# Optimization experiments

Hardware: AMD Instinct MI355X
Metric: run time of the kernel (lower is better)

Reference implementation:

```python
import jax, jax.numpy as jnp
import numpy as np

B_, S_, D_ = 2, 1024, 1024
EXPAND = 2
D_INNER = EXPAND * D_            # 2048
HEADDIM = 64
NHEADS = D_INNER // HEADDIM      # 32
D_STATE = 64
NGROUPS = 1
D_CONV = 4
CONV_DIM = D_INNER + 2 * NGROUPS * D_STATE      # 2176
D_IN_PROJ = 2 * D_INNER + 2 * NGROUPS * D_STATE + NHEADS  # 4256
H_MLP = 8 * D_                   # GatedMLP fc_1 out (scale * d_model)


def setup_inputs() -> dict:
    key = jax.random.key(0)
    ks = jax.random.split(key, 12)
    n = lambda k, shp, s=0.02: jax.random.normal(k, shp, dtype=jnp.float32) * s
    return {
        "x": jax.random.normal(ks[0], (B_, S_, D_), dtype=jnp.float32),
        "in_proj_w": n(ks[1], (D_IN_PROJ, D_)),
        "conv_w": n(ks[2], (CONV_DIM, D_CONV), 0.2),
        "conv_b": jnp.zeros((CONV_DIM,), jnp.float32),
        "dt_bias": jax.random.normal(ks[3], (NHEADS,), dtype=jnp.float32) * 0.5 - 2.0,
        "A_log": jnp.log(1.0 + 15.0 * jax.random.uniform(ks[4], (NHEADS,), dtype=jnp.float32)),
        "D": jax.random.normal(ks[5], (NHEADS,), dtype=jnp.float32) * 0.1 + 1.0,
        "ssm_norm_w": jnp.ones((D_INNER,), jnp.float32),
        "out_proj_w": n(ks[6], (D_, D_INNER)),
        "rms_w": jnp.ones((D_,), jnp.float32),
        "fc1_w": n(ks[7], (H_MLP, D_)),
        "fc2_w": n(ks[8], (D_, H_MLP // 2)),
    }


def _rms(x, w, eps=1e-5):
    return x * jax.lax.rsqrt(jnp.mean(x * x, axis=-1, keepdims=True) + eps) * w


def _mamba(x, in_proj_w, conv_w, conv_b, dt_bias, A_log, D, ssm_norm_w, out_proj_w):
    b, s, _ = x.shape
    zxbcdt = x @ in_proj_w.T                         # [b,s,D_IN_PROJ]
    z = zxbcdt[..., :D_INNER]
    xBC = zxbcdt[..., D_INNER:D_INNER + CONV_DIM]
    dt_raw = zxbcdt[..., -NHEADS:]
    # causal depthwise conv1d + SiLU
    xc = jnp.pad(jnp.transpose(xBC, (0, 2, 1)), ((0, 0), (0, 0), (D_CONV - 1, 0)))
    xc = jax.lax.conv_general_dilated(xc, conv_w[:, None, :], (1,), 'VALID',
                                      feature_group_count=CONV_DIM,
                                      dimension_numbers=('NCH', 'OIH', 'NCH'))
    xBC = jax.nn.silu(jnp.transpose(xc, (0, 2, 1)) + conv_b)
    xs = xBC[..., :D_INNER].reshape(b, s, NHEADS, HEADDIM)
    Bm = xBC[..., D_INNER:D_INNER + D_STATE]         # [b,s,n] (ngroups=1)
    Cm = xBC[..., D_INNER + D_STATE:]
    dt = jax.nn.softplus(dt_raw + dt_bias)           # [b,s,h]
    dA = jnp.exp(dt * (-jnp.exp(A_log)))             # [b,s,h]
    dtx = dt[..., None] * xs                          # [b,s,h,p]

    def step(h, inp):
        dA_t, dtx_t, B_t, C_t = inp
        h = h * dA_t[:, :, None, None] + jnp.einsum('bhp,bn->bhpn', dtx_t, B_t)
        y = jnp.einsum('bhpn,bn->bhp', h, C_t)
        return h, y

    h0 = jnp.zeros((b, NHEADS, HEADDIM, D_STATE), x.dtype)
    _, y = jax.lax.scan(step, h0, (jnp.transpose(dA, (1, 0, 2)),
                                   jnp.transpose(dtx, (1, 0, 2, 3)),
                                   jnp.transpose(Bm, (1, 0, 2)),
                                   jnp.transpose(Cm, (1, 0, 2))))
    y = jnp.transpose(y, (1, 0, 2, 3)) + D[None, None, :, None] * xs
    y = y.reshape(b, s, D_INNER) * jax.nn.silu(z)    # gated
    y = _rms(y, ssm_norm_w)
    return y @ out_proj_w.T


def reference(x, in_proj_w, conv_w, conv_b, dt_bias, A_log, D, ssm_norm_w,
              out_proj_w, rms_w, fc1_w, fc2_w):
    # x = x + mamba(x)
    x = x + _mamba(x, in_proj_w, conv_w, conv_b, dt_bias, A_log, D, ssm_norm_w, out_proj_w)
    # x = x + GatedMLP(RMSNorm(x))
    xn = _rms(x, rms_w)
    h1 = xn @ fc1_w.T
    a, g = jnp.split(h1, 2, axis=-1)
    m = (a * jax.nn.silu(g)) @ fc2_w.T
    return x + m
```

## Files before the change

### kernel.cpp

```cpp
#include <hip/hip_runtime.h>
#include <math.h>

typedef unsigned short u16;
typedef __attribute__((ext_vector_type(8))) __bf16 bf16x8;
typedef __attribute__((ext_vector_type(4))) float f32x4;
typedef __attribute__((ext_vector_type(4))) u16 u16x4;
typedef __attribute__((ext_vector_type(8))) u16 u16x8;
typedef __attribute__((ext_vector_type(4))) float float4v;

constexpr int kS = 1024;
constexpr int kD = 1024;
constexpr int kDinner = 2048;
constexpr int kHeads = 32;
constexpr int kConvDim = 2176;
constexpr int kDproj = 4256;
constexpr int kDprojPad = 4352;
constexpr int kRows = 2048;
constexpr int kHmlp = 8192;
constexpr int kHhalf = 4096;
constexpr int kL = 64;
constexpr int kNC = 16;

__device__ __forceinline__ float bf2f(u16 u) {
    return __builtin_bit_cast(float, (unsigned int)u << 16);
}
__device__ __forceinline__ u16 f2bf(float f) {
    unsigned int u = __builtin_bit_cast(unsigned int, f);
    u += 0x7fffu + ((u >> 16) & 1u);
    return (u16)(u >> 16);
}
__device__ __forceinline__ float silu_(float x) { return x / (1.f + __expf(-x)); }

__device__ __forceinline__ void gld16(const u16* g, u16* l) {
    __builtin_amdgcn_global_load_lds(
        (const __attribute__((address_space(1))) void*)g,
        (__attribute__((address_space(3))) void*)l, 16, 0, 0);
}

constexpr int kB1 = kRows * kD / 4;
constexpr int kB2 = kB1 + kDprojPad * kD / 4;
constexpr int kB3 = kB2 + kD * kDinner / 4;
constexpr int kB4 = kB3 + kHmlp * kD / 4;
constexpr int kB5 = kB4 + kD * kHhalf / 4;
__global__ __launch_bounds__(256)
void cast_all_kernel(const float* __restrict__ x, const float* __restrict__ w1,
                     const float* __restrict__ w2, const float* __restrict__ w3,
                     const float* __restrict__ w4, u16* __restrict__ xbf,
                     u16* __restrict__ w1bf, u16* __restrict__ w2bf,
                     u16* __restrict__ w3bf, u16* __restrict__ w4bf) {
    int i = blockIdx.x * 256 + threadIdx.x;
    const float* src;
    u16* dst;
    int j;
    if (i < kB1) {
        j = i; src = x; dst = xbf;
    } else if (i < kB2) {
        j = i - kB1;
        int e = j * 4, row = e >> 10, col = e & 1023;
        u16x4 o = {0, 0, 0, 0};
        if (row < kDproj) {
            float4v v = *(const float4v*)(w1 + (size_t)row * kD + col);
            o.x = f2bf(v.x); o.y = f2bf(v.y); o.z = f2bf(v.z); o.w = f2bf(v.w);
        }
        ((u16x4*)w1bf)[j] = o;
        return;
    } else if (i < kB3) {
        j = i - kB2; src = w2; dst = w2bf;
    } else if (i < kB4) {
        j = i - kB3;
        int e = j * 4, row = e >> 10, col4 = (e & 1023) >> 2;
        int p = (row < kHhalf) ? row : row - kHhalf;
        int permrow = (p >> 4) * 32 + (p & 15) + ((row < kHhalf) ? 0 : 16);
        float4v v = ((const float4v*)w3)[j];
        u16x4 o;
        o.x = f2bf(v.x); o.y = f2bf(v.y); o.z = f2bf(v.z); o.w = f2bf(v.w);
        ((u16x4*)w3bf)[permrow * 256 + col4] = o;
        return;
    } else {
        j = i - kB4; src = w4; dst = w4bf;
    }
    float4v v = ((const float4v*)src)[j];
    u16x4 o;
    o.x = f2bf(v.x); o.y = f2bf(v.y); o.z = f2bf(v.z); o.w = f2bf(v.w);
    ((u16x4*)dst)[j] = o;
}

template <bool OUT_BF16, bool GATED = false>
__global__ __launch_bounds__(256)
void gemm_bt(const u16* __restrict__ A, const u16* __restrict__ W,
             void* __restrict__ Cout, const float* __restrict__ resid,
             int M, int N, int K) {
    __shared__ u16 As[2][128 * 32];
    __shared__ u16 Bs[2][128 * 32];
    const int tid = threadIdx.x;
    const int lane = tid & 63;
    const int w = __builtin_amdgcn_readfirstlane(tid >> 6);
    const int wm = w >> 1, wn = w & 1;
    const int bm = blockIdx.y * 128;
    const int bn = blockIdx.x * 128;
    const int z = blockIdx.z;
    const int Kchunk = K / gridDim.z;
    const int k0 = z * Kchunk;

    f32x4 acc[4][4];
#pragma unroll
    for (int i = 0; i < 4; i++)
#pragma unroll
        for (int j = 0; j < 4; j++) acc[i][j] = {0.f, 0.f, 0.f, 0.f};

    const int srow = lane >> 2;
    const int scol = (lane & 3) * 8;
    const u16* gA = A + (size_t)(bm + w * 32 + srow) * K + k0 + scol;
    const u16* gB = W + (size_t)(bn + w * 32 + srow) * K + k0 + scol;
    const size_t rstep = (size_t)16 * K;

    const int sbase0 = (w * 32) * 32;
    const int sbase1 = (w * 32 + 16) * 32;
    const int fra = (lane & 15) * 32 + (lane >> 4) * 8;

    gld16(gA, &As[0][sbase0]);
    gld16(gA + rstep, &As[0][sbase1]);
    gld16(gB, &Bs[0][sbase0]);
    gld16(gB + rstep, &Bs[0][sbase1]);

    const int nk = Kchunk >> 5;
    for (int i = 0; i < nk; i++) {
        const int cur = i & 1, nxt = cur ^ 1;
        __syncthreads();
        if (i + 1 < nk) {
            int kt2 = (i + 1) * 32;
            gld16(gA + kt2, &As[nxt][sbase0]);
            gld16(gA + kt2 + rstep, &As[nxt][sbase1]);
            gld16(gB + kt2, &Bs[nxt][sbase0]);
            gld16(gB + kt2 + rstep, &Bs[nxt][sbase1]);
        }
        bf16x8 av[4], bv[4];
#pragma unroll
        for (int mi = 0; mi < 4; mi++)
            av[mi] = *(const bf16x8*)&As[cur][(wm * 64 + mi * 16) * 32 + fra];
#pragma unroll
        for (int ni = 0; ni < 4; ni++)
            bv[ni] = *(const bf16x8*)&Bs[cur][(wn * 64 + ni * 16) * 32 + fra];
#pragma unroll
        for (int mi = 0; mi < 4; mi++)
#pragma unroll
            for (int ni = 0; ni < 4; ni++)
                acc[mi][ni] = __builtin_amdgcn_mfma_f32_16x16x32_bf16(av[mi], bv[ni], acc[mi][ni], 0, 0, 0);
    }

    const int rb = bm + wm * 64 + ((lane >> 4) << 2);
    const int cb = bn + wn * 64 + (lane & 15);
    if (GATED) {
        u16* Cb = (u16*)Cout;
        const int NG = N >> 1;
        const int gc0 = ((bn + wn * 64) >> 1) + (lane & 15);
#pragma unroll
        for (int mi = 0; mi < 4; mi++) {
#pragma unroll
            for (int p = 0; p < 2; p++) {
#pragma unroll
                for (int r = 0; r < 4; r++) {
                    float a = acc[mi][2 * p][r];
                    float g = acc[mi][2 * p + 1][r];
                    Cb[(size_t)(rb + mi * 16 + r) * NG + gc0 + p * 16] =
                        f2bf(a * silu_(g));
                }
            }
        }
        return;
    }
    float* Cf = (float*)Cout + (size_t)z * M * N;
    u16* Cb = (u16*)Cout;
#pragma unroll
    for (int mi = 0; mi < 4; mi++) {
#pragma unroll
        for (int ni = 0; ni < 4; ni++) {
#pragma unroll
            for (int r = 0; r < 4; r++) {
                size_t offo = (size_t)(rb + mi * 16 + r) * N + (cb + ni * 16);
                float v = acc[mi][ni][r];
                if (resid) v += resid[offo];
                if (OUT_BF16) Cb[offo] = f2bf(v);
                else Cf[offo] = v;
            }
        }
    }
}

#define VMCNT6 asm volatile("s_waitcnt vmcnt(6)" ::: "memory")
#define VMCNT0 asm volatile("s_waitcnt vmcnt(0)" ::: "memory")

__global__ __launch_bounds__(512, 2)
void gemm256_gated(const u16* __restrict__ A, const u16* __restrict__ W,
                   u16* __restrict__ Cout, int M, int N, int K) {
    __shared__ u16 lds[2][2][2][2][4096];
    const int tid = threadIdx.x;
    const int lane = tid & 63;
    const int w = __builtin_amdgcn_readfirstlane(tid >> 6);
    const int wm = w >> 2;
    const int wn = w & 3;
    const int wnh = wn >> 1, wnl = wn & 1;

    const int lin = blockIdx.x;
    const int xcd = lin & 7, j = lin >> 3;
    const int bm = (((xcd >> 2) << 2) + (j & 3)) << 8;
    const int bn = (((xcd & 3) << 3) + (j >> 2)) << 8;

    const int rst = tid >> 2, sst = tid & 3;
    const int vst = (((rst >> 1) & 1) << 1) | ((rst >> 2) & 1);
    const u16* gA0 = A + (size_t)(bm + rst) * K + ((sst ^ vst) << 3);
    const u16* gB0 = W + (size_t)(bn + rst) * K + ((sst ^ vst) << 3);
    const size_t hstep = (size_t)128 * K;
    const int wq512 = w * 512;

    const int r0a = lane & 15, slot = lane >> 4;
    const int v2a = (((r0a >> 1) & 1) << 1) | ((r0a >> 2) & 1);
    const int fro = r0a * 32 + ((slot ^ v2a) << 3);

    f32x4 acc[8][4];
#pragma unroll
    for (int i = 0; i < 8; i++)
#pragma unroll
        for (int j_ = 0; j_ < 4; j_++) acc[i][j_] = {0.f, 0.f, 0.f, 0.f};
    bf16x8 bv[4];
    const int nt = K >> 6;

#define STAGE(d, mat, kh, kt)                                               \
    { const u16* g_ = ((mat) ? gB0 : gA0) + (size_t)(kt) * 64 + (kh) * 32;  \
      gld16(g_, &lds[d][mat][0][kh][wq512]);                                \
      gld16(g_ + hstep, &lds[d][mat][1][kh][wq512]); }

#define LDA_FRAG(dst, d, kh, mfb)                                           \
    _Pragma("unroll") for (int i_ = 0; i_ < 4; i_++)                        \
        dst[i_] = *(const bf16x8*)&lds[d][0][wm][kh][((mfb) + i_) * 512 + fro];

#define LDB_FRAG(d, kh)                                                     \
    _Pragma("unroll") for (int i_ = 0; i_ < 4; i_++)                        \
        bv[i_] = *(const bf16x8*)&lds[d][1][wnh][kh][wnl * 2048 + i_ * 512 + fro];

#define PHASE_TAIL(g4, ...)                                                 \
    __builtin_amdgcn_s_barrier();                                           \
    asm volatile("s_waitcnt lgkmcnt(0)" ::: "memory");                      \
    __builtin_amdgcn_s_setprio(1);                                          \
    _Pragma("unroll") for (int i_ = 0; i_ < 4; i_++)                        \
        _Pragma("unroll") for (int n_ = 0; n_ < 4; n_++)                    \
            acc[(g4) * 4 + i_][n_] = __builtin_amdgcn_mfma_f32_16x16x32_bf16( \
                av[i_], bv[n_], acc[(g4) * 4 + i_][n_], 0, 0, 0);           \
    __builtin_amdgcn_s_setprio(0);                                          \
    __VA_ARGS__;                                                            \
    __builtin_amdgcn_s_barrier();

#define TILE(T, D)                                                          \
    {                                             \
      { bf16x8 av[4]; LDB_FRAG(D, 0); LDA_FRAG(av, D, 0, 0);                \
        if ((T) + 1 < nt) STAGE(D ^ 1, 0, 1, (T) + 1);                      \
        PHASE_TAIL(0, ((void)0)) }                                          \
                                                  \
      { bf16x8 av[4]; LDA_FRAG(av, D, 0, 4);                                \
        if ((T) + 2 < nt) STAGE(D, 1, 0, (T) + 2);                          \
        PHASE_TAIL(1, ((void)0)) }                                          \
                                                  \
      { bf16x8 av[4]; LDB_FRAG(D, 1); LDA_FRAG(av, D, 1, 0);                \
        if ((T) + 2 < nt) STAGE(D, 0, 0, (T) + 2);                          \
        PHASE_TAIL(0, ((void)0)) }                                          \
                \
      { bf16x8 av[4]; LDA_FRAG(av, D, 1, 4);                                \
        if ((T) + 2 < nt) STAGE(D, 1, 1, (T) + 2);                          \
        PHASE_TAIL(1, if ((T) + 2 < nt) { VMCNT6; }                         \
                      else if ((T) + 1 < nt) { VMCNT0; }) }                 \
    }

    STAGE(0, 1, 0, 0);
    STAGE(0, 0, 0, 0);
    STAGE(0, 1, 1, 0);
    STAGE(0, 0, 1, 0);
    STAGE(1, 1, 0, 1);
    STAGE(1, 0, 0, 1);
    STAGE(1, 1, 1, 1);
    VMCNT6;
    __builtin_amdgcn_s_barrier();

    for (int tt = 0; tt < nt; tt += 2) {
        TILE(tt, 0)
        TILE(tt + 1, 1)
    }

#undef TILE
#undef PHASE_TAIL
#undef LDB_FRAG
#undef LDA_FRAG
#undef STAGE

    __syncthreads();
    u16* cst = (u16*)&lds[0][0][0][0][0];
    constexpr int LDE = 136;
#pragma unroll
    for (int mf = 0; mf < 8; mf++) {
#pragma unroll
        for (int p = 0; p < 2; p++) {
#pragma unroll
            for (int r = 0; r < 4; r++) {
                float a = acc[mf][2 * p][r];
                float g = acc[mf][2 * p + 1][r];
                cst[(wm * 128 + mf * 16 + slot * 4 + r) * LDE +
                    wn * 32 + p * 16 + r0a] = f2bf(a * silu_(g));
            }
        }
    }
    __syncthreads();
    const int NG = N >> 1;
#pragma unroll
    for (int k = 0; k < 8; k++) {
        int ch = k * 512 + tid;
        int row = ch >> 4, c8 = (ch & 15) * 8;
        *(u16x8*)(Cout + (size_t)(bm + row) * NG + (bn >> 1) + c8) =
            *(const u16x8*)&cst[row * LDE + c8];
    }
}

__global__ __launch_bounds__(256)
void splitk_reduce_kernel(const float* __restrict__ Cp, const float* __restrict__ resid,
                          float* __restrict__ out, int mn4) {
    int i = blockIdx.x * 256 + threadIdx.x;
    if (i >= mn4) return;
    constexpr size_t MN = (size_t)kRows * kD;
    float4v s0 = ((const float4v*)Cp)[i];
    float4v s1 = ((const float4v*)(Cp + MN))[i];
    float4v s2 = ((const float4v*)(Cp + 2 * MN))[i];
    float4v s3 = ((const float4v*)(Cp + 3 * MN))[i];
    float4v r = ((const float4v*)resid)[i];
    float4v o;
    o.x = s0.x + s1.x + s2.x + s3.x + r.x;
    o.y = s0.y + s1.y + s2.y + s3.y + r.y;
    o.z = s0.z + s1.z + s2.z + s3.z + r.z;
    o.w = s0.w + s1.w + s2.w + s3.w + r.w;
    ((float4v*)out)[i] = o;
}

__global__ __launch_bounds__(256)
void reduce_rms_kernel(const float* __restrict__ Cp, const float* __restrict__ resid,
                       float* __restrict__ x2, const float* __restrict__ rmsw,
                       u16* __restrict__ xnbf) {
    const int row = blockIdx.x;
    const int tid = threadIdx.x;
    constexpr size_t MN = (size_t)kRows * kD;
    size_t i = (size_t)row * (kD / 4) + tid;
    float4v s0 = ((const float4v*)Cp)[i];
    float4v s1 = ((const float4v*)(Cp + MN))[i];
    float4v s2 = ((const float4v*)(Cp + 2 * MN))[i];
    float4v s3 = ((const float4v*)(Cp + 3 * MN))[i];
    float4v r = ((const float4v*)resid)[i];
    float4v v;
    v.x = s0.x + s1.x + s2.x + s3.x + r.x;
    v.y = s0.y + s1.y + s2.y + s3.y + r.y;
    v.z = s0.z + s1.z + s2.z + s3.z + r.z;
    v.w = s0.w + s1.w + s2.w + s3.w + r.w;
    ((float4v*)x2)[i] = v;
    float ss = v.x * v.x + v.y * v.y + v.z * v.z + v.w * v.w;
#pragma unroll
    for (int off = 32; off > 0; off >>= 1) ss += __shfl_down(ss, off);
    __shared__ float red[4];
    int wv = tid >> 6, lane = tid & 63;
    if (lane == 0) red[wv] = ss;
    __syncthreads();
    ss = red[0] + red[1] + red[2] + red[3];
    float rstd = rsqrtf(ss * (1.f / kD) + 1e-5f);
    float4v wv4 = ((const float4v*)rmsw)[tid];
    u16x4 o;
    o.x = f2bf(v.x * rstd * wv4.x);
    o.y = f2bf(v.y * rstd * wv4.y);
    o.z = f2bf(v.z * rstd * wv4.z);
    o.w = f2bf(v.w * rstd * wv4.w);
    ((u16x4*)xnbf)[i] = o;
}

__global__ __launch_bounds__(256)
void convdt_kernel(const u16* __restrict__ zxbf, const float* __restrict__ convw,
                   const float* __restrict__ convb, u16* __restrict__ xsbf,
                   float* __restrict__ BCf, const float* __restrict__ dt_bias,
                   float* __restrict__ dtf) {
    int c = blockIdx.x * 256 + threadIdx.x;
    int row = blockIdx.y;
    if (c >= kConvDim + kHeads) return;
    if (c < kConvDim) {
        int s = row & (kS - 1);
        float acc = convb[c];
#pragma unroll
        for (int j = 0; j < 4; j++) {
            int sj = s - 3 + j;
            if (sj >= 0)
                acc += bf2f(zxbf[(size_t)(row - 3 + j) * kDprojPad + kDinner + c]) * convw[c * 4 + j];
        }
        float v = silu_(acc);
        if (c < kDinner) xsbf[(size_t)row * kDinner + c] = f2bf(v);
        else BCf[(size_t)row * 128 + (c - kDinner)] = v;
    } else {
        int h = c - kConvDim;
        float raw = bf2f(zxbf[(size_t)row * kDprojPad + (kDinner + kConvDim) + h]) + dt_bias[h];
        float dt = (raw > 20.f) ? raw : log1pf(__expf(raw));
        dtf[(size_t)row * kHeads + h] = dt;
    }
}

__global__ __launch_bounds__(256)
void scan_chunk_kernel(const u16* __restrict__ xsbf, const float* __restrict__ BCf,
                       const float* __restrict__ dtf, const float* __restrict__ A_log,
                       const float* __restrict__ Dv, u16* __restrict__ ysbf,
                       float* __restrict__ Pf, float* __restrict__ Scf) {
    constexpr int LDT = 72;
    __shared__ __align__(16) char smem[65280];
    u16* Chi  = (u16*)(smem);
    u16* Clo  = (u16*)(smem + 9216);
    u16* Bhi  = (u16*)(smem + 18432);
    u16* Blo  = (u16*)(smem + 27648);
    u16* BThi = (u16*)(smem + 36864);
    u16* BTlo = (u16*)(smem + 46080);
    u16* xT   = (u16*)(smem + 55296);
    float* laS  = (float*)(smem + 64512);
    float* dtS  = (float*)(smem + 64768);
    float* wscS = (float*)(smem + 65024);
    u16* Mhi  = Clo;
    u16* Mlo  = Bhi;
    u16* ybuf = Chi;

    const int c = blockIdx.x, h = blockIdx.y, b = blockIdx.z;
    const int tid = threadIdx.x;
    const int lane = tid & 63;
    const int w = __builtin_amdgcn_readfirstlane(tid >> 6);
    const int row0 = b * kS + c * kL;
    const int frow = lane & 15;
    const int fk = (lane >> 4) * 8;
    const int q4 = (lane >> 4) * 4;
    const int w16 = w * 16;

#pragma unroll
    for (int k = 0; k < 8; k++) {
        int e4 = k * 256 + tid;
        int t = e4 >> 5, col = (e4 & 31) * 4;
        float4v v = *(const float4v*)(BCf + (size_t)(row0 + t) * 128 + col);
        u16x4 hi, lo;
        hi.x = f2bf(v.x); lo.x = f2bf(v.x - bf2f(hi.x));
        hi.y = f2bf(v.y); lo.y = f2bf(v.y - bf2f(hi.y));
        hi.z = f2bf(v.z); lo.z = f2bf(v.z - bf2f(hi.z));
        hi.w = f2bf(v.w); lo.w = f2bf(v.w - bf2f(hi.w));
        int cc = col & 63;
        u16* dh = (col < 64) ? Bhi : Chi;
        u16* dl = (col < 64) ? Blo : Clo;
        *(u16x4*)&dh[t * LDT + cc] = hi;
        *(u16x4*)&dl[t * LDT + cc] = lo;
    }
#pragma unroll
    for (int k = 0; k < 2; k++) {
        int e8 = k * 256 + tid;
        int t = e8 >> 3, p8 = (e8 & 7) * 8;
        u16x8 xv = *(const u16x8*)(xsbf + (size_t)(row0 + t) * kDinner + h * 64 + p8);
#pragma unroll
        for (int j = 0; j < 8; j++) xT[(p8 + j) * LDT + t] = xv[j];
    }
    if (tid < 64) {
        float d = dtf[(size_t)(row0 + tid) * kHeads + h];
        dtS[tid] = d;
        float cs = d;
#pragma unroll
        for (int off = 1; off < 64; off <<= 1) {
            float o = __shfl_up(cs, off);
            if (lane >= off) cs += o;
        }
        float A_h = __expf(A_log[h]);
        float la = -A_h * cs;
        laS[tid] = la;
        Pf[(size_t)(row0 + tid) * kHeads + h] = __expf(la);
        float la63 = __shfl(la, 63);
        wscS[tid] = d * __expf(la63 - la);
    }
    __syncthreads();

    f32x4 accG[4];
#pragma unroll
    for (int i = 0; i < 4; i++) accG[i] = {0.f, 0.f, 0.f, 0.f};
#pragma unroll
    for (int kb = 0; kb < 2; kb++) {
        bf16x8 ch = *(const bf16x8*)&Chi[(w16 + frow) * LDT + kb * 32 + fk];
        bf16x8 cl = *(const bf16x8*)&Clo[(w16 + frow) * LDT + kb * 32 + fk];
#pragma unroll
        for (int nt = 0; nt < 4; nt++) {
            if (nt <= w) {
                bf16x8 bh = *(const bf16x8*)&Bhi[(nt * 16 + frow) * LDT + kb * 32 + fk];
                bf16x8 bl = *(const bf16x8*)&Blo[(nt * 16 + frow) * LDT + kb * 32 + fk];
                accG[nt] = __builtin_amdgcn_mfma_f32_16x16x32_bf16(ch, bh, accG[nt], 0, 0, 0);
                accG[nt] = __builtin_amdgcn_mfma_f32_16x16x32_bf16(ch, bl, accG[nt], 0, 0, 0);
                accG[nt] = __builtin_amdgcn_mfma_f32_16x16x32_bf16(cl, bh, accG[nt], 0, 0, 0);
            }
        }
    }
#pragma unroll
    for (int k = 0; k < 16; k++) {
        int e = k * 256 + tid;
        int s = e >> 6, n = e & 63;
        BThi[n * LDT + s] = Bhi[s * LDT + n];
        BTlo[n * LDT + s] = Blo[s * LDT + n];
    }
    __syncthreads();

    f32x4 la4 = *(const f32x4*)&laS[w16 + q4];
#pragma unroll
    for (int nt = 0; nt < 4; nt++) {
        int s = nt * 16 + frow;
        float las = laS[s], dts = dtS[s];
#pragma unroll
        for (int r = 0; r < 4; r++) {
            int t = w16 + q4 + r;
            float f = 0.f;
            if (nt <= w && s <= t)
                f = dts * __expf(la4[r] - las) * accG[nt][r];
            u16 mh = f2bf(f);
            u16 ml = f2bf(f - bf2f(mh));
            Mhi[t * LDT + s] = mh;
            Mlo[t * LDT + s] = ml;
        }
    }

    f32x4 accY[4];
#pragma unroll
    for (int i = 0; i < 4; i++) accY[i] = {0.f, 0.f, 0.f, 0.f};
#pragma unroll
    for (int kb = 0; kb < 2; kb++) {
        bf16x8 mh = *(const bf16x8*)&Mhi[(w16 + frow) * LDT + kb * 32 + fk];
        bf16x8 ml = *(const bf16x8*)&Mlo[(w16 + frow) * LDT + kb * 32 + fk];
#pragma unroll
        for (int nt = 0; nt < 4; nt++) {
            bf16x8 xv = *(const bf16x8*)&xT[(nt * 16 + frow) * LDT + kb * 32 + fk];
            accY[nt] = __builtin_amdgcn_mfma_f32_16x16x32_bf16(mh, xv, accY[nt], 0, 0, 0);
            accY[nt] = __builtin_amdgcn_mfma_f32_16x16x32_bf16(ml, xv, accY[nt], 0, 0, 0);
        }
    }

    f32x4 accS[4];
#pragma unroll
    for (int i = 0; i < 4; i++) accS[i] = {0.f, 0.f, 0.f, 0.f};
#pragma unroll
    for (int kb = 0; kb < 2; kb++) {
        u16x8 xu = __builtin_bit_cast(u16x8, *(const bf16x8*)&xT[(w16 + frow) * LDT + kb * 32 + fk]);
        f32x4 w0v = *(const f32x4*)&wscS[kb * 32 + fk];
        f32x4 w1v = *(const f32x4*)&wscS[kb * 32 + fk + 4];
        u16x8 xh, xl;
#pragma unroll
        for (int j = 0; j < 8; j++) {
            float wv = (j < 4) ? w0v[j] : w1v[j - 4];
            float f = bf2f(xu[j]) * wv;
            u16 hh = f2bf(f);
            xh[j] = hh;
            xl[j] = f2bf(f - bf2f(hh));
        }
        bf16x8 xwh = __builtin_bit_cast(bf16x8, xh);
        bf16x8 xwl = __builtin_bit_cast(bf16x8, xl);
#pragma unroll
        for (int nt = 0; nt < 4; nt++) {
            bf16x8 bh = *(const bf16x8*)&BThi[(nt * 16 + frow) * LDT + kb * 32 + fk];
            bf16x8 bl = *(const bf16x8*)&BTlo[(nt * 16 + frow) * LDT + kb * 32 + fk];
            accS[nt] = __builtin_amdgcn_mfma_f32_16x16x32_bf16(xwh, bh, accS[nt], 0, 0, 0);
            accS[nt] = __builtin_amdgcn_mfma_f32_16x16x32_bf16(xwh, bl, accS[nt], 0, 0, 0);
            accS[nt] = __builtin_amdgcn_mfma_f32_16x16x32_bf16(xwl, bh, accS[nt], 0, 0, 0);
        }
    }

    const float Dh = Dv[h];
    const int bhc = (b * 32 + h) * kNC + c;
    float* Sb = Scf + (size_t)bhc * 4096;
#pragma unroll
    for (int nt = 0; nt < 4; nt++) {
#pragma unroll
        for (int r = 0; r < 4; r++) {
            int t = w16 + q4 + r;
            int pc = nt * 16 + frow;
            float y = accY[nt][r] + Dh * bf2f(xT[pc * LDT + t]);
            ybuf[t * 64 + pc] = f2bf(y);
            Sb[t * 64 + pc] = accS[nt][r];
        }
    }
    __syncthreads();
#pragma unroll
    for (int k = 0; k < 2; k++) {
        int e8 = k * 256 + tid;
        int t = e8 >> 3, col8 = (e8 & 7) * 8;
        *(u16x8*)(ysbf + (size_t)(row0 + t) * kDinner + h * 64 + col8) =
            *(u16x8*)&ybuf[t * 64 + col8];
    }
}

__global__ __launch_bounds__(256)
void chunk_state_kernel(const float* __restrict__ Scf, const float* __restrict__ Pf,
                        float* __restrict__ Hinf) {
    const int bh = blockIdx.x;
    const int b = bh >> 5, h = bh & 31;
    const int tid = threadIdx.x;
    float hreg[16];
#pragma unroll
    for (int k = 0; k < 16; k++) hreg[k] = 0.f;
    for (int c = 0; c < kNC - 1; c++) {
        float Q = Pf[(size_t)(b * kS + c * kL + kL - 1) * kHeads + h];
        size_t sbase = (size_t)(bh * kNC + c) * 4096;
        size_t dbase = (size_t)(bh * kNC + c + 1) * 4096;
#pragma unroll
        for (int k = 0; k < 16; k++) {
            float s = Scf[sbase + k * 256 + tid];
            hreg[k] = Q * hreg[k] + s;
            Hinf[dbase + k * 256 + tid] = hreg[k];
        }
    }
}

__global__ __launch_bounds__(256)
void chunk_corr_kernel(const float* __restrict__ Hinf, const float* __restrict__ BCf,
                       const float* __restrict__ Pf, u16* __restrict__ ysbf) {
    const int c = blockIdx.x + 1;
    const int h = blockIdx.y, b = blockIdx.z;
    const int tid = threadIdx.x;
    const int lane = tid & 63, wq = tid >> 6;
    __shared__ float Hin_lds[64 * 65];
    __shared__ float C_lds[kL * 64];
    const int bh = b * 32 + h;
    const size_t hbase = (size_t)(bh * kNC + c) * 4096;
#pragma unroll
    for (int k = 0; k < 16; k++) {
        int e = k * 256 + tid;
        Hin_lds[(e >> 6) * 65 + (e & 63)] = Hinf[hbase + e];
    }
    const int row0 = b * kS + c * kL;
#pragma unroll
    for (int k = 0; k < 4; k++) {
        int e4 = k * 256 + tid;
        int t = e4 >> 4, n4 = (e4 & 15) * 4;
        *(float4v*)&C_lds[t * 64 + n4] =
            *(const float4v*)(BCf + (size_t)(row0 + t) * 128 + 64 + n4);
    }
    __syncthreads();

    float hr[64];
#pragma unroll
    for (int n = 0; n < 64; n++) hr[n] = Hin_lds[lane * 65 + n];

    for (int tt = 0; tt < 16; tt++) {
        int t = wq * 16 + tt;
        float corr = 0.f;
#pragma unroll
        for (int n4 = 0; n4 < 16; n4++) {
            float4v cv = *(const float4v*)&C_lds[t * 64 + n4 * 4];
            corr += cv.x * hr[n4 * 4] + cv.y * hr[n4 * 4 + 1] +
                    cv.z * hr[n4 * 4 + 2] + cv.w * hr[n4 * 4 + 3];
        }
        float Pt = Pf[(size_t)(row0 + t) * kHeads + h];
        size_t yoff = (size_t)(row0 + t) * kDinner + h * 64 + lane;
        ysbf[yoff] = f2bf(bf2f(ysbf[yoff]) + Pt * corr);
    }
}

__global__ __launch_bounds__(256)
void gatenorm_kernel(const u16* __restrict__ ysbf, const u16* __restrict__ zxbf,
                     const float* __restrict__ normw, u16* __restrict__ ybf) {
    const int row = blockIdx.x;
    const int tid = threadIdx.x;
    float v[8];
    float ss = 0.f;
#pragma unroll
    for (int i = 0; i < 8; i++) {
        int idx = i * 256 + tid;
        float y = bf2f(ysbf[(size_t)row * kDinner + idx]);
        float z = bf2f(zxbf[(size_t)row * kDprojPad + idx]);
        v[i] = y * silu_(z);
        ss += v[i] * v[i];
    }
#pragma unroll
    for (int off = 32; off > 0; off >>= 1) ss += __shfl_down(ss, off);
    __shared__ float red[4];
    int wv = tid >> 6, lane = tid & 63;
    if (lane == 0) red[wv] = ss;
    __syncthreads();
    ss = red[0] + red[1] + red[2] + red[3];
    float rstd = rsqrtf(ss * (1.f / kDinner) + 1e-5f);
#pragma unroll
    for (int i = 0; i < 8; i++) {
        int idx = i * 256 + tid;
        ybf[(size_t)row * kDinner + idx] = f2bf(v[i] * rstd * normw[idx]);
    }
}

extern "C" void kernel_launch(void* const* d_in, const int* in_sizes, int n_in,
                              void* d_out, int out_size, void* d_ws, size_t ws_size,
                              hipStream_t stream) {
    const float* x         = (const float*)d_in[0];
    const float* in_proj_w = (const float*)d_in[1];
    const float* conv_w    = (const float*)d_in[2];
    const float* conv_b    = (const float*)d_in[3];
    const float* dt_bias   = (const float*)d_in[4];
    const float* A_log     = (const float*)d_in[5];
    const float* Dvec      = (const float*)d_in[6];
    const float* ssm_norm_w= (const float*)d_in[7];
    const float* out_proj_w= (const float*)d_in[8];
    const float* rms_w     = (const float*)d_in[9];
    const float* fc1_w     = (const float*)d_in[10];
    const float* fc2_w     = (const float*)d_in[11];
    float* out = (float*)d_out;

    char* ws = (char*)d_ws;
    size_t off = 0;
    auto alloc = [&](size_t bytes) -> void* {
        void* p = ws + off;
        off += (bytes + 255) & ~(size_t)255;
        return p;
    };
    u16*   xbf  = (u16*)alloc((size_t)kRows * kD * 2);
    u16*   w1bf = (u16*)alloc((size_t)kDprojPad * kD * 2);
    u16*   w2bf = (u16*)alloc((size_t)kD * kDinner * 2);
    u16*   w3bf = (u16*)alloc((size_t)kHmlp * kD * 2);
    u16*   w4bf = (u16*)alloc((size_t)kD * kHhalf * 2);
    u16*   zxbf = (u16*)alloc((size_t)kRows * kDprojPad * 2);
    u16*   xsbf = (u16*)alloc((size_t)kRows * kDinner * 2);
    float* BCf  = (float*)alloc((size_t)kRows * 128 * 4);
    float* dtf  = (float*)alloc((size_t)kRows * kHeads * 4);
    float* Pf   = (float*)alloc((size_t)kRows * kHeads * 4);
    u16*   ysbf = (u16*)alloc((size_t)kRows * kDinner * 2);
    u16*   ybf  = (u16*)alloc((size_t)kRows * kDinner * 2);
    float* x2   = (float*)alloc((size_t)kRows * kD * 4);
    u16*   xnbf = (u16*)alloc((size_t)kRows * kD * 2);
    u16*   h1bf = (u16*)alloc((size_t)kRows * kHmlp * 2);
    u16*   gbf  = (u16*)alloc((size_t)kRows * kHhalf * 2);
    float* Scf  = (float*)gbf;
    float* Hinf = (float*)h1bf;
    float* Cp   = (float*)h1bf;
    (void)ws_size; (void)in_sizes; (void)n_in; (void)out_size;

    cast_all_kernel<<<kB5 / 256, 256, 0, stream>>>(
        x, in_proj_w, out_proj_w, fc1_w, fc2_w, xbf, w1bf, w2bf, w3bf, w4bf);

    gemm_bt<true><<<dim3(kDprojPad / 128, kRows / 128, 1), 256, 0, stream>>>(
        xbf, w1bf, zxbf, nullptr, kRows, kDprojPad, kD);

    convdt_kernel<<<dim3((kConvDim + kHeads + 255) / 256, kRows), 256, 0, stream>>>(
        zxbf, conv_w, conv_b, xsbf, BCf, dt_bias, dtf);

    scan_chunk_kernel<<<dim3(kNC, kHeads, 2), 256, 0, stream>>>(
        xsbf, BCf, dtf, A_log, Dvec, ysbf, Pf, Scf);
    chunk_state_kernel<<<64, 256, 0, stream>>>(Scf, Pf, Hinf);
    chunk_corr_kernel<<<dim3(kNC - 1, kHeads, 2), 256, 0, stream>>>(Hinf, BCf, Pf, ysbf);

    gatenorm_kernel<<<kRows, 256, 0, stream>>>(ysbf, zxbf, ssm_norm_w, ybf);

    gemm_bt<false><<<dim3(kD / 128, kRows / 128, 4), 256, 0, stream>>>(
        ybf, w2bf, Cp, nullptr, kRows, kD, kDinner);
    reduce_rms_kernel<<<kRows, 256, 0, stream>>>(Cp, x, x2, rms_w, xnbf);

    gemm256_gated<<<dim3((kRows >> 8) * (kHmlp >> 8)), 512, 0, stream>>>(
        xnbf, w3bf, gbf, kRows, kHmlp, kD);

    gemm_bt<false><<<dim3(kD / 128, kRows / 128, 4), 256, 0, stream>>>(
        gbf, w4bf, Cp, nullptr, kRows, kD, kHhalf);
    splitk_reduce_kernel<<<(kRows * kD / 4 + 255) / 256, 256, 0, stream>>>(
        Cp, x2, out, kRows * kD / 4);
}
```

Before: 344.9 us.

## Use 4-wave 128x128 warp tiles in gated GEMM; parallelize chunk-state over elements

The 256x256 gated fc1 GEMM now runs with 256 threads (4 waves in a 2x2 arrangement) instead of 512 (8 waves). Each wave computes a 128x128 sub-tile with 8x8 MFMA accumulators and loads 8 B fragments per k-half, which raises per-wave reuse and cuts LDS fragment reads per MFMA. Global staging issues four 16-byte loads per thread and the vmcnt thresholds are adjusted to match. The risk is higher register pressure, lower occupancy and less latency hiding with fewer waves. Separately, chunk_state_kernel is spread over a 16x larger grid with one element per thread, so the sequential inter-chunk recurrence runs on more CUs in parallel.

```diff
diff --git a/kernel.cpp b/kernel.cpp
--- a/kernel.cpp
+++ b/kernel.cpp
@@ -187,19 +187,18 @@
     }
 }
 
-#define VMCNT6 asm volatile("s_waitcnt vmcnt(6)" ::: "memory")
-#define VMCNT0 asm volatile("s_waitcnt vmcnt(0)" ::: "memory")
-
-__global__ __launch_bounds__(512, 2)
+#define VMCNT12 asm volatile("s_waitcnt vmcnt(12)" ::: "memory")
+#define VMCNT0  asm volatile("s_waitcnt vmcnt(0)" ::: "memory")
+
+__global__ __launch_bounds__(256, 1)
 void gemm256_gated(const u16* __restrict__ A, const u16* __restrict__ W,
                    u16* __restrict__ Cout, int M, int N, int K) {
     __shared__ u16 lds[2][2][2][2][4096];
     const int tid = threadIdx.x;
     const int lane = tid & 63;
     const int w = __builtin_amdgcn_readfirstlane(tid >> 6);
-    const int wm = w >> 2;
-    const int wn = w & 3;
-    const int wnh = wn >> 1, wnl = wn & 1;
+    const int wm = w >> 1;
+    const int wn = w & 1;
 
     const int lin = blockIdx.x;
     const int xcd = lin & 7, j = lin >> 3;
@@ -210,63 +209,65 @@
     const int vst = (((rst >> 1) & 1) << 1) | ((rst >> 2) & 1);
     const u16* gA0 = A + (size_t)(bm + rst) * K + ((sst ^ vst) << 3);
     const u16* gB0 = W + (size_t)(bn + rst) * K + ((sst ^ vst) << 3);
-    const size_t hstep = (size_t)128 * K;
+    const size_t h64 = (size_t)64 * K;
     const int wq512 = w * 512;
 
     const int r0a = lane & 15, slot = lane >> 4;
     const int v2a = (((r0a >> 1) & 1) << 1) | ((r0a >> 2) & 1);
     const int fro = r0a * 32 + ((slot ^ v2a) << 3);
 
-    f32x4 acc[8][4];
+    f32x4 acc[8][8];
 #pragma unroll
     for (int i = 0; i < 8; i++)
 #pragma unroll
-        for (int j_ = 0; j_ < 4; j_++) acc[i][j_] = {0.f, 0.f, 0.f, 0.f};
-    bf16x8 bv[4];
+        for (int j_ = 0; j_ < 8; j_++) acc[i][j_] = {0.f, 0.f, 0.f, 0.f};
+    bf16x8 bv[8];
     const int nt = K >> 6;
 
 #define STAGE(d, mat, kh, kt)                                               \
     { const u16* g_ = ((mat) ? gB0 : gA0) + (size_t)(kt) * 64 + (kh) * 32;  \
-      gld16(g_, &lds[d][mat][0][kh][wq512]);                                \
-      gld16(g_ + hstep, &lds[d][mat][1][kh][wq512]); }
+      gld16(g_,            &lds[d][mat][0][kh][wq512]);                     \
+      gld16(g_ + h64,      &lds[d][mat][0][kh][2048 + wq512]);              \
+      gld16(g_ + 2 * h64,  &lds[d][mat][1][kh][wq512]);                     \
+      gld16(g_ + 3 * h64,  &lds[d][mat][1][kh][2048 + wq512]); }
 
 #define LDA_FRAG(dst, d, kh, mfb)                                           \
     _Pragma("unroll") for (int i_ = 0; i_ < 4; i_++)                        \
         dst[i_] = *(const bf16x8*)&lds[d][0][wm][kh][((mfb) + i_) * 512 + fro];
 
 #define LDB_FRAG(d, kh)                                                     \
-    _Pragma("unroll") for (int i_ = 0; i_ < 4; i_++)                        \
-        bv[i_] = *(const bf16x8*)&lds[d][1][wnh][kh][wnl * 2048 + i_ * 512 + fro];
-
-#define PHASE_TAIL(g4, ...)                                                 \
+    _Pragma("unroll") for (int i_ = 0; i_ < 8; i_++)                        \
+        bv[i_] = *(const bf16x8*)&lds[d][1][wn][kh][i_ * 512 + fro];
+
+#define PHASE_TAIL(mfb, ...)                                                \
     __builtin_amdgcn_s_barrier();                                           \
     asm volatile("s_waitcnt lgkmcnt(0)" ::: "memory");                      \
     __builtin_amdgcn_s_setprio(1);                                          \
     _Pragma("unroll") for (int i_ = 0; i_ < 4; i_++)                        \
-        _Pragma("unroll") for (int n_ = 0; n_ < 4; n_++)                    \
-            acc[(g4) * 4 + i_][n_] = __builtin_amdgcn_mfma_f32_16x16x32_bf16( \
-                av[i_], bv[n_], acc[(g4) * 4 + i_][n_], 0, 0, 0);           \
+        _Pragma("unroll") for (int n_ = 0; n_ < 8; n_++)                    \
+            acc[(mfb) + i_][n_] = __builtin_amdgcn_mfma_f32_16x16x32_bf16(  \
+                av[i_], bv[n_], acc[(mfb) + i_][n_], 0, 0, 0);              \
     __builtin_amdgcn_s_setprio(0);                                          \
     __VA_ARGS__;                                                            \
     __builtin_amdgcn_s_barrier();
 
 #define TILE(T, D)                                                          \
-    {                                             \
+    {                                                  \
       { bf16x8 av[4]; LDB_FRAG(D, 0); LDA_FRAG(av, D, 0, 0);                \
         if ((T) + 1 < nt) STAGE(D ^ 1, 0, 1, (T) + 1);                      \
         PHASE_TAIL(0, ((void)0)) }                                          \
-                                                  \
+                                                       \
       { bf16x8 av[4]; LDA_FRAG(av, D, 0, 4);                                \
         if ((T) + 2 < nt) STAGE(D, 1, 0, (T) + 2);                          \
-        PHASE_TAIL(1, ((void)0)) }                                          \
-                                                  \
+        PHASE_TAIL(4, ((void)0)) }                                          \
+                                                       \
       { bf16x8 av[4]; LDB_FRAG(D, 1); LDA_FRAG(av, D, 1, 0);                \
         if ((T) + 2 < nt) STAGE(D, 0, 0, (T) + 2);                          \
         PHASE_TAIL(0, ((void)0)) }                                          \
-                \
+                     \
       { bf16x8 av[4]; LDA_FRAG(av, D, 1, 4);                                \
         if ((T) + 2 < nt) STAGE(D, 1, 1, (T) + 2);                          \
-        PHASE_TAIL(1, if ((T) + 2 < nt) { VMCNT6; }                         \
+        PHASE_TAIL(4, if ((T) + 2 < nt) { VMCNT12; }                        \
                       else if ((T) + 1 < nt) { VMCNT0; }) }                 \
     }
 
@@ -277,7 +278,7 @@
     STAGE(1, 1, 0, 1);
     STAGE(1, 0, 0, 1);
     STAGE(1, 1, 1, 1);
-    VMCNT6;
+    VMCNT12;
     __builtin_amdgcn_s_barrier();
 
     for (int tt = 0; tt < nt; tt += 2) {
@@ -297,21 +298,21 @@
 #pragma unroll
     for (int mf = 0; mf < 8; mf++) {
 #pragma unroll
-        for (int p = 0; p < 2; p++) {
+        for (int p = 0; p < 4; p++) {
 #pragma unroll
             for (int r = 0; r < 4; r++) {
                 float a = acc[mf][2 * p][r];
                 float g = acc[mf][2 * p + 1][r];
                 cst[(wm * 128 + mf * 16 + slot * 4 + r) * LDE +
-                    wn * 32 + p * 16 + r0a] = f2bf(a * silu_(g));
+                    wn * 64 + p * 16 + r0a] = f2bf(a * silu_(g));
             }
         }
     }
     __syncthreads();
     const int NG = N >> 1;
 #pragma unroll
-    for (int k = 0; k < 8; k++) {
-        int ch = k * 512 + tid;
+    for (int k = 0; k < 16; k++) {
+        int ch = k * 256 + tid;
         int row = ch >> 4, c8 = (ch & 15) * 8;
         *(u16x8*)(Cout + (size_t)(bm + row) * NG + (bn >> 1) + c8) =
             *(const u16x8*)&cst[row * LDE + c8];
@@ -593,20 +594,12 @@
                         float* __restrict__ Hinf) {
     const int bh = blockIdx.x;
     const int b = bh >> 5, h = bh & 31;
-    const int tid = threadIdx.x;
-    float hreg[16];
-#pragma unroll
-    for (int k = 0; k < 16; k++) hreg[k] = 0.f;
+    const int eo = blockIdx.y * 256 + threadIdx.x;
+    float hreg = 0.f;
     for (int c = 0; c < kNC - 1; c++) {
         float Q = Pf[(size_t)(b * kS + c * kL + kL - 1) * kHeads + h];
-        size_t sbase = (size_t)(bh * kNC + c) * 4096;
-        size_t dbase = (size_t)(bh * kNC + c + 1) * 4096;
-#pragma unroll
-        for (int k = 0; k < 16; k++) {
-            float s = Scf[sbase + k * 256 + tid];
-            hreg[k] = Q * hreg[k] + s;
-            Hinf[dbase + k * 256 + tid] = hreg[k];
-        }
+        hreg = Q * hreg + Scf[(size_t)(bh * kNC + c) * 4096 + eo];
+        Hinf[(size_t)(bh * kNC + c + 1) * 4096 + eo] = hreg;
     }
 }
 
@@ -741,7 +734,7 @@
 
     scan_chunk_kernel<<<dim3(kNC, kHeads, 2), 256, 0, stream>>>(
         xsbf, BCf, dtf, A_log, Dvec, ysbf, Pf, Scf);
-    chunk_state_kernel<<<64, 256, 0, stream>>>(Scf, Pf, Hinf);
+    chunk_state_kernel<<<dim3(64, 16), 256, 0, stream>>>(Scf, Pf, Hinf);
     chunk_corr_kernel<<<dim3(kNC - 1, kHeads, 2), 256, 0, stream>>>(Hinf, BCf, Pf, ysbf);
 
     gatenorm_kernel<<<kRows, 256, 0, stream>>>(ysbf, zxbf, ssm_norm_w, ybf);
@@ -750,7 +743,7 @@
         ybf, w2bf, Cp, nullptr, kRows, kD, kDinner);
     reduce_rms_kernel<<<kRows, 256, 0, stream>>>(Cp, x, x2, rms_w, xnbf);
 
-    gemm256_gated<<<dim3((kRows >> 8) * (kHmlp >> 8)), 512, 0, stream>>>(
+    gemm256_gated<<<dim3((kRows >> 8) * (kHmlp >> 8)), 256, 0, stream>>>(
         xnbf, w3bf, gbf, kRows, kHmlp, kD);
 
     gemm_bt<false><<<dim3(kD / 128, kRows / 128, 4), 256, 0, stream>>>(
```

New measurement: 420.2 us. +21.8%, slower.
